# Performance work log

Hardware: AMD Instinct MI355X
Metric: run time of the kernel (lower is better)

## Reference

```python
import jax, jax.numpy as jnp
import numpy as np

B, N_NODE, N_TOK = 8, 512, 8
N_PATHS, PATH_LEN = 256, 64
VOCAB, H = 50000, 256


def gru_dir(x, w_ih, w_hh, b_ih, b_hh):
    # x: [batch, T, H_in] -> [batch, T, H]; PyTorch GRU gate math
    xw = jnp.einsum('bti,gi->btg', x, w_ih) + b_ih  # precompute input-side gates
    h0 = jnp.zeros((x.shape[0], w_hh.shape[1]), x.dtype)
    def step(h, xt):
        gh = h @ w_hh.T + b_hh
        xr, xz, xn = jnp.split(xt, 3, -1)
        hr, hz, hn = jnp.split(gh, 3, -1)
        r = jax.nn.sigmoid(xr + hr)
        z = jax.nn.sigmoid(xz + hz)
        n = jnp.tanh(xn + r * hn)
        h_new = (1.0 - z) * n + z * h
        return h_new, h_new
    _, ys = jax.lax.scan(step, h0, jnp.swapaxes(xw, 0, 1))
    return jnp.swapaxes(ys, 0, 1)


def gru_bidir(x, wf_ih, wf_hh, bf_ih, bf_hh, wb_ih, wb_hh, bb_ih, bb_hh):
    f = gru_dir(x, wf_ih, wf_hh, bf_ih, bf_hh)
    b = jnp.flip(gru_dir(jnp.flip(x, 1), wb_ih, wb_hh, bb_ih, bb_hh), 1)
    return jnp.concatenate([f, b], -1)


def setup_inputs():
    key = jax.random.key(0)
    ks = jax.random.split(key, 18)
    g = lambda k, s: jax.random.normal(k, s, jnp.float32) * 0.06
    return {
        'nodes': jax.random.randint(ks[0], (B, N_NODE, N_TOK), 0, VOCAB),
        'paths': jax.random.randint(ks[1], (B, N_PATHS, PATH_LEN), 0, N_NODE + 1),
        'emb': g(ks[2], (VOCAB, H)),
        'wf_ih': g(ks[3], (3 * H, H)), 'wf_hh': g(ks[4], (3 * H, H)),
        'bf_ih': g(ks[5], (3 * H,)), 'bf_hh': g(ks[6], (3 * H,)),
        'wb_ih': g(ks[7], (3 * H, H)), 'wb_hh': g(ks[8], (3 * H, H)),
        'bb_ih': g(ks[9], (3 * H,)), 'bb_hh': g(ks[10], (3 * H,)),
        'w_transit': g(ks[11], (2 * H, H)), 'b_transit': g(ks[12], (2 * H,)),
        'w_rank': g(ks[13], (2 * H, 2 * H + 1)), 'b_rank': g(ks[14], (2 * H,)),
        'w_h': g(ks[15], (H, 2 * H)), 'b_h': g(ks[16], (H,)),
    }


def reference(nodes, paths, emb, wf_ih, wf_hh, bf_ih, bf_hh, wb_ih, wb_hh, bb_ih, bb_hh, w_transit, b_transit, w_rank, b_rank, w_h, b_h):
    gru = (wf_ih, wf_hh, bf_ih, bf_hh, wb_ih, wb_hh, bb_ih, bb_hh)
    x = jnp.max(emb[nodes], axis=2)                 # [B, N_NODE, H] token max-pool
    base_v = gru_bidir(x, *gru)                     # [B, N_NODE, 2H]
    x_pad = jnp.concatenate([x, jnp.zeros((B, 1, H), x.dtype)], axis=1)
    gathered = jax.vmap(lambda xp, p: xp[p])(x_pad, paths)        # [B, P, L, H]
    nx = gru_bidir(gathered.reshape(B * N_PATHS, PATH_LEN, H), *gru)
    nx = nx.reshape(B, N_PATHS, PATH_LEN, 2 * H)
    # extra rank feature: 1/(path_index+1), broadcast over path positions
    rank = (1.0 / (jnp.arange(N_PATHS, dtype=x.dtype) + 1.0))[None, :, None, None]
    rank = jnp.broadcast_to(rank, (B, N_PATHS, PATH_LEN, 1))
    nx = jnp.concatenate([nx, rank], -1) @ w_rank.T + b_rank      # rank_proj
    p_flat = paths.reshape(B, -1)
    v_flat = nx.reshape(B, N_PATHS * PATH_LEN, 2 * H)
    def pool(pf, vf, xb):
        # scatter-max per node id; id N_NODE is the padding row and is dropped
        vmax = jnp.full((N_NODE + 1, 2 * H), -jnp.inf, vf.dtype).at[pf].max(vf)
        has = jnp.zeros((N_NODE + 1,), bool).at[pf].set(True)
        fallback = xb @ w_transit.T + b_transit
        return jnp.where(has[:N_NODE, None], vmax[:N_NODE], fallback)
    v = jax.vmap(pool)(p_flat, v_flat, x)           # [B, N_NODE, 2H]
    all_v = base_v + v
    last_state = jnp.max(all_v, axis=1) @ w_h.T + b_h             # h_proj branch (GRU -> not tuple)
    return all_v, last_state
```

## Files before the change

### kernel.cpp

```cpp
#include <hip/hip_runtime.h>


#define HH 256
#define NNODE 512
#define PLEN 64

typedef __attribute__((ext_vector_type(8))) short short8;
typedef __attribute__((ext_vector_type(4))) float f32x4;
typedef unsigned short ushort_t;
typedef __attribute__((address_space(1))) const void* gas_t;
typedef __attribute__((address_space(3))) void* las_t;

__device__ __forceinline__ f32x4 mfma16(short8 a, short8 b, f32x4 c) {
    return __builtin_amdgcn_mfma_f32_16x16x32_bf16(a, b, c, 0, 0, 0);
}
__device__ __forceinline__ ushort_t f2bf(float f) {
    unsigned u = __float_as_uint(f);
    u += 0x7fffu + ((u >> 16) & 1u);
    return (ushort_t)(u >> 16);
}
__device__ __forceinline__ float bf2f(ushort_t s) {
    return __uint_as_float(((unsigned)s) << 16);
}
__device__ __forceinline__ float sigm(float x) {
    return __builtin_amdgcn_rcpf(1.f + __expf(-x));
}
__device__ __forceinline__ float tanh_(float x) {
    return 1.f - 2.f * __builtin_amdgcn_rcpf(__expf(2.f * x) + 1.f);
}
__device__ __forceinline__ unsigned fkey(float f) {
    unsigned u = __float_as_uint(f);
    return (u & 0x80000000u) ? ~u : (u | 0x80000000u);
}
__device__ __forceinline__ float fdec(unsigned k) {
    unsigned u = (k & 0x80000000u) ? (k ^ 0x80000000u) : ~k;
    return __uint_as_float(u);
}

__device__ __forceinline__ int xw3_remap(int c) {
    const int dir = c >= 768;
    const int cd = c - dir * 768;
    const int g = cd >> 8, cc = cd & 255;
    const int w2 = cc >> 5, within = cc & 31;
    return dir * 768 + w2 * 96 + (within >> 1) * 6 + g * 2 + (within & 1);
}

__global__ void k_embed(const int* __restrict__ nodes, const float* __restrict__ emb,
                        float* __restrict__ x, ushort_t* __restrict__ xbf)
{
    const int bn = blockIdx.x, h = threadIdx.x;
    const int* nd = nodes + bn * 8;
    float m = -3.4e38f;
#pragma unroll
    for (int k = 0; k < 8; ++k)
        m = fmaxf(m, emb[(size_t)nd[k] * HH + h]);
    x[(size_t)bn * HH + h] = m;
    xbf[(size_t)bn * HH + h] = f2bf(m);
}

__global__ void k_pack(const float* __restrict__ wf_ih, const float* __restrict__ wf_hh,
                       const float* __restrict__ bf_ih, const float* __restrict__ bf_hh,
                       const float* __restrict__ wb_ih, const float* __restrict__ wb_hh,
                       const float* __restrict__ bb_ih, const float* __restrict__ bb_hh,
                       const float* __restrict__ w_rank,
                       ushort_t* __restrict__ whhp, ushort_t* __restrict__ wih_bt,
                       ushort_t* __restrict__ wr_bt, float* __restrict__ rank_l,
                       float* __restrict__ bias2, ushort_t* __restrict__ xw3)
{
    int i = blockIdx.x * 256 + threadIdx.x;
    if (i < 393216) {
        const int e = i & 7, l = (i >> 3) & 63;
        int c = i >> 9;
        const int n = c & 1; c >>= 1;
        const int g = c % 3; c /= 3;
        const int kt = c & 7; c >>= 3;
        const int w2 = c & 7;
        const int dir = c >> 3;
        const float* whh = dir ? wb_hh : wf_hh;
        whhp[i] = f2bf(whh[(g * 256 + w2 * 32 + 2 * (l & 15) + n) * 256 +
                           kt * 32 + (l >> 4) * 8 + e]);
        return;
    }
    i -= 393216;
    if (i < 393216) {
        const int n = i >> 8, k = i & 255;
        const float* wih = (n < 768) ? wf_ih : wb_ih;
        wih_bt[i] = f2bf(wih[(n % 768) * 256 + k]);
        return;
    }
    i -= 393216;
    if (i < 262144) { wr_bt[i] = f2bf(w_rank[(i >> 9) * 513 + (i & 511)]); return; }
    i -= 262144;
    if (i < 512) { rank_l[i] = w_rank[i * 513 + 512]; return; }
    i -= 512;
    if (i < 1536) {
        const int c = i;
        const int dir = c >= 768;
        const int cd = c - dir * 768;
        const int g = cd >> 8;
        const float bi = dir ? bb_ih[cd] : bf_ih[cd];
        const float bh = (g < 2) ? (dir ? bb_hh[cd] : bf_hh[cd]) : 0.f;
        bias2[c] = bi + bh;
        xw3[(size_t)4096 * 1536 + xw3_remap(c)] = f2bf(bi + bh);
    }
}

template<int KD>
__device__ __forceinline__ void gemm_loop(const ushort_t* __restrict__ A,
                                          const ushort_t* __restrict__ Bt,
                                          ushort_t* al, ushort_t* bl,
                                          int bm, int bn, f32x4 acc[4][4])
{
    const int tid = threadIdx.x, w = tid >> 6, l = tid & 63;
    const int lm = l & 15, lh = l >> 4;
    const int wm = w >> 1, wn = w & 1;
    const int lr = l >> 3, lc = (l & 7) * 8;
    for (int k0 = 0; k0 < KD; k0 += 64) {
#pragma unroll
        for (int i = 0; i < 4; ++i) {
            const int c = w * 4 + i;
            const ushort_t* ga = A + (size_t)(bm + c * 8 + lr) * KD + k0 + lc;
            const ushort_t* gb = Bt + (size_t)(bn + c * 8 + lr) * KD + k0 + lc;
            __builtin_amdgcn_global_load_lds((gas_t)ga, (las_t)(al + c * 512), 16, 0, 0);
            __builtin_amdgcn_global_load_lds((gas_t)gb, (las_t)(bl + c * 512), 16, 0, 0);
        }
        __syncthreads();
#pragma unroll
        for (int kt = 0; kt < 2; ++kt) {
            short8 af[4], bfr[4];
            const int ko = kt * 32 + lh * 8;
#pragma unroll
            for (int m = 0; m < 4; ++m)
                af[m] = *(const short8*)(al + (wm * 64 + m * 16 + lm) * 64 + ko);
#pragma unroll
            for (int n = 0; n < 4; ++n)
                bfr[n] = *(const short8*)(bl + (wn * 64 + n * 16 + lm) * 64 + ko);
#pragma unroll
            for (int m = 0; m < 4; ++m)
#pragma unroll
                for (int n = 0; n < 4; ++n)
                    acc[m][n] = mfma16(af[m], bfr[n], acc[m][n]);
        }
        __syncthreads();
    }
}

__global__ void __launch_bounds__(256, 2)
k_gemm_xw(const ushort_t* __restrict__ xbf, const ushort_t* __restrict__ wih_bt,
          const float* __restrict__ bias2, ushort_t* __restrict__ xw3)
{
    __shared__ __align__(16) ushort_t al[128 * 64], bl[128 * 64];
    f32x4 acc[4][4] = {};
    const int bm = blockIdx.y * 128, bn = blockIdx.x * 128;
    gemm_loop<256>(xbf, wih_bt, al, bl, bm, bn, acc);
    const int tid = threadIdx.x, w = tid >> 6, l = tid & 63;
    const int lm = l & 15, lh = l >> 4, wm = w >> 1, wn = w & 1;
#pragma unroll
    for (int m = 0; m < 4; ++m)
#pragma unroll
        for (int rr = 0; rr < 4; ++rr) {
            const int row = bm + wm * 64 + m * 16 + lh * 4 + rr;
#pragma unroll
            for (int n = 0; n < 4; ++n) {
                const int col = bn + wn * 64 + n * 16 + lm;
                xw3[(size_t)row * 1536 + xw3_remap(col)] = f2bf(acc[m][n][rr] + bias2[col]);
            }
        }
}

template<bool IS_BASE>
__device__ __forceinline__ void scan_run(int dir, int sg, int tid,
    const ushort_t* __restrict__ xw3, const ushort_t* __restrict__ whhp,
    const float* __restrict__ bhh, ushort_t (*hl)[8192], const int* idr,
    ushort_t* __restrict__ nx, float* __restrict__ base_v)
{
    const int w = tid >> 6, l = tid & 63;
    const int lm = l & 15, lh = l >> 4;
    const int nsteps = IS_BASE ? NNODE : PLEN;

    short8 Bf[8][3][2];
    {
        const ushort_t* wp = whhp + (size_t)(dir * 8 + w) * 24576 + l * 8;
#pragma unroll
        for (int kt = 0; kt < 8; ++kt)
#pragma unroll
            for (int g = 0; g < 3; ++g)
#pragma unroll
                for (int n = 0; n < 2; ++n) {
                    short8 v = *(const short8*)(wp + (kt * 6 + g * 2 + n) * 512);
                    asm volatile("" : "+a"(v));
                    Bf[kt][g][n] = v;
                }
    }
    const float bn0 = bhh[512 + w * 32 + lm * 2];
    const float bn1 = bhh[512 + w * 32 + lm * 2 + 1];

    __syncthreads();
    for (int i = tid; i < 4096; i += 512) hl[0][i] = 0;
    __syncthreads();

    int cur = 0;
    for (int step = 0; step < nsteps; ++step) {
        const int t = dir ? (nsteps - 1 - step) : step;
        uint3 gv[4];
#pragma unroll
        for (int ri = 0; ri < 4; ++ri) {
            const int sq = lh * 4 + ri;
            const int row = IS_BASE ? ((sq < 8) ? ((sq << 9) + t) : 4096)
                                    : idr[(sq << 6) + t];
            gv[ri] = *(const uint3*)((const char*)xw3 +
                (size_t)row * 3072 + dir * 1536 + w * 192 + lm * 12);
        }
        f32x4 acc[3][2] = {};
        const char* hb = (const char*)hl[cur];
#pragma unroll
        for (int kt = 0; kt < 8; ++kt) {
            const short8 a = *(const short8*)(hb + lm * 512 +
                ((kt * 64 + lh * 16) ^ ((lm & 7) << 4)));
#pragma unroll
            for (int g = 0; g < 3; ++g)
#pragma unroll
                for (int n = 0; n < 2; ++n)
                    acc[g][n] = mfma16(a, Bf[kt][g][n], acc[g][n]);
        }
        ushort_t* hn_ = hl[cur ^ 1];
#pragma unroll
        for (int ri = 0; ri < 4; ++ri) {
            const int sq = lh * 4 + ri;
            const unsigned hv = *(const unsigned*)(hb + sq * 512 +
                ((w * 64 + lm * 4) ^ ((sq & 7) << 4)));
            unsigned hpack = 0;
            float hs0 = 0.f, hs1 = 0.f;
#pragma unroll
            for (int n = 0; n < 2; ++n) {
                const float xr = bf2f((ushort_t)(n ? (gv[ri].x >> 16) : (gv[ri].x & 0xffffu)));
                const float xz = bf2f((ushort_t)(n ? (gv[ri].y >> 16) : (gv[ri].y & 0xffffu)));
                const float xn = bf2f((ushort_t)(n ? (gv[ri].z >> 16) : (gv[ri].z & 0xffffu)));
                const float hov = bf2f((ushort_t)(n ? (hv >> 16) : (hv & 0xffffu)));
                const float rr = sigm(acc[0][n][ri] + xr);
                const float zz = sigm(acc[1][n][ri] + xz);
                const float nn = tanh_(xn + rr * (acc[2][n][ri] + (n ? bn1 : bn0)));
                const float h = (1.f - zz) * nn + zz * hov;
                if (n) hs1 = h; else hs0 = h;
                hpack |= ((unsigned)f2bf(h)) << (n * 16);
            }
            *(unsigned*)((char*)hn_ + sq * 512 + ((w * 64 + lm * 4) ^ ((sq & 7) << 4))) = hpack;
            if (IS_BASE) {
                if (sq < 8)
                    *(float2*)(base_v + ((size_t)(sq * NNODE + t)) * 512 +
                               dir * 256 + w * 32 + lm * 2) = make_float2(hs0, hs1);
            } else {
                *(unsigned*)((char*)nx + (((size_t)((sg * 16 + sq) * PLEN + t)) * 512 +
                    dir * 256 + w * 32 + lm * 2) * 2) = hpack;
            }
        }
        __syncthreads();
        cur ^= 1;
    }
}

__global__ void __launch_bounds__(512)
k_scan(const int* __restrict__ paths, const ushort_t* __restrict__ xw3,
       const ushort_t* __restrict__ whhp,
       const float* __restrict__ bf_hh, const float* __restrict__ bb_hh,
       const ushort_t* __restrict__ wr_bt, const float* __restrict__ b_rank,
       const float* __restrict__ rank_l,
       ushort_t* __restrict__ nx, float* __restrict__ base_v,
       unsigned* __restrict__ keys)
{
    __shared__ __align__(16) ushort_t hl[2][8192];
    __shared__ __align__(16) ushort_t al[12288], bl[12288];
    __shared__ int idr[1024];
    const int tid = threadIdx.x;
    const int w = tid >> 6, l = tid & 63;
    const int lm = l & 15, lh = l >> 4;

    if (blockIdx.x < 2) {
        scan_run<true>((int)blockIdx.x, 0, tid, xw3, whhp,
                       blockIdx.x ? bb_hh : bf_hh, hl, nullptr, nx, base_v);
        return;
    }
    const int sg = (int)blockIdx.x - 2;
    for (int i = tid; i < 1024; i += 512) {
        const int s = sg * 16 + (i >> 6), t = i & 63;
        const int id = paths[(s << 6) + t];
        idr[i] = (id < NNODE) ? (((s >> 8) << 9) + id) : 4096;
    }
    scan_run<false>(0, sg, tid, xw3, whhp, bf_hh, hl, idr, nx, base_v);
    scan_run<false>(1, sg, tid, xw3, whhp, bb_hh, hl, idr, nx, base_v);

    __threadfence_block();
    __syncthreads();
    const int wm = w >> 2, wn = w & 3;
#pragma unroll 1
    for (int job = 0; job < 32; ++job) {
        const int mt = job >> 2, ntile = job & 3;
        const size_t ar0 = (size_t)sg * 1024 + mt * 128;
        const int n0 = ntile * 128;
        f32x4 racc[4][2] = {};
        for (int k0 = 0; k0 < 512; k0 += 64) {
#pragma unroll
            for (int i = 0; i < 2; ++i) {
                const int c = w * 128 + i * 64 + l;
                const int row = c >> 3, j = c & 7;
                const int jp = j ^ (row & 7);
                __builtin_amdgcn_global_load_lds(
                    (gas_t)(nx + (ar0 + row) * 512 + k0 + jp * 8),
                    (las_t)(al + c * 8), 16, 0, 0);
                __builtin_amdgcn_global_load_lds(
                    (gas_t)(wr_bt + (size_t)(n0 + row) * 512 + k0 + jp * 8),
                    (las_t)(bl + c * 8), 16, 0, 0);
            }
            __syncthreads();
#pragma unroll
            for (int kt = 0; kt < 2; ++kt) {
                short8 av[4], bv[2];
#pragma unroll
                for (int m = 0; m < 4; ++m) {
                    const int r = wm * 64 + m * 16 + lm;
                    av[m] = *(const short8*)((const char*)al + r * 128 +
                            ((kt * 64 + lh * 16) ^ ((r & 7) << 4)));
                }
#pragma unroll
                for (int n = 0; n < 2; ++n) {
                    const int r = wn * 32 + n * 16 + lm;
                    bv[n] = *(const short8*)((const char*)bl + r * 128 +
                            ((kt * 64 + lh * 16) ^ ((r & 7) << 4)));
                }
#pragma unroll
                for (int m = 0; m < 4; ++m)
#pragma unroll
                    for (int n = 0; n < 2; ++n)
                        racc[m][n] = mfma16(av[m], bv[n], racc[m][n]);
            }
            __syncthreads();
        }
#pragma unroll
        for (int m = 0; m < 4; ++m)
#pragma unroll
            for (int rr = 0; rr < 4; ++rr) {
                const size_t grow = ar0 + wm * 64 + m * 16 + lh * 4 + rr;
                const int id = paths[grow];
                const float rv = __builtin_amdgcn_rcpf((float)(((grow >> 6) & 255) + 1));
                unsigned* kp = keys + (((grow >> 14) * 513 + id) << 9);
#pragma unroll
                for (int n = 0; n < 2; ++n) {
                    const int col = n0 + wn * 32 + n * 16 + lm;
                    const float v = racc[m][n][rr] + b_rank[col] + rank_l[col] * rv;
                    if (id < NNODE) {
                        const unsigned key = fkey(v);
                        if (key > kp[col]) atomicMax(kp + col, key);
                    }
                }
            }
    }
}

__global__ void k_merge(const unsigned* __restrict__ keys, const float* __restrict__ base_v,
                        const float* __restrict__ x, const float* __restrict__ w_transit,
                        const float* __restrict__ b_transit, float* __restrict__ out0)
{
    const int blk = blockIdx.x;
    const int b = blk >> 9, n = blk & 511;
    const int tid = threadIdx.x;
#pragma unroll
    for (int h = 0; h < 2; ++h) {
        const int o = tid + h * 256;
        const unsigned k = keys[((size_t)(b * 513 + n)) * 512 + o];
        float v;
        if (k) {
            v = fdec(k);
        } else {
            float a = b_transit[o];
            const float* wt = w_transit + o * HH;
            const float* xr = x + ((size_t)(b * NNODE + n)) * HH;
            for (int i = 0; i < HH; ++i) a += xr[i] * wt[i];
            v = a;
        }
        const size_t oi = ((size_t)(b * NNODE + n)) * 512 + o;
        out0[oi] = base_v[oi] + v;
    }
}

__global__ void k_last(const float* __restrict__ out0, const float* __restrict__ w_h,
                       const float* __restrict__ b_h, float* __restrict__ out1)
{
    __shared__ float m[512];
    const int b = blockIdx.x, tid = threadIdx.x;
#pragma unroll
    for (int h = 0; h < 2; ++h) {
        const int o = tid + h * 256;
        float mm = -3.4e38f;
        for (int n = 0; n < NNODE; ++n)
            mm = fmaxf(mm, out0[((size_t)(b * NNODE + n)) * 512 + o]);
        m[o] = mm;
    }
    __syncthreads();
    float a = b_h[tid];
    const float* wr = w_h + tid * 512;
    for (int j = 0; j < 512; ++j) a += m[j] * wr[j];
    out1[b * HH + tid] = a;
}

extern "C" void kernel_launch(void* const* d_in, const int* in_sizes, int n_in,
                              void* d_out, int out_size, void* d_ws, size_t ws_size,
                              hipStream_t stream)
{
    (void)in_sizes; (void)n_in; (void)out_size; (void)ws_size;
    const int* nodes = (const int*)d_in[0];
    const int* paths = (const int*)d_in[1];
    const float* emb = (const float*)d_in[2];
    const float* wf_ih = (const float*)d_in[3];
    const float* wf_hh = (const float*)d_in[4];
    const float* bf_ih = (const float*)d_in[5];
    const float* bf_hh = (const float*)d_in[6];
    const float* wb_ih = (const float*)d_in[7];
    const float* wb_hh = (const float*)d_in[8];
    const float* bb_ih = (const float*)d_in[9];
    const float* bb_hh = (const float*)d_in[10];
    const float* w_transit = (const float*)d_in[11];
    const float* b_transit = (const float*)d_in[12];
    const float* w_rank = (const float*)d_in[13];
    const float* b_rank = (const float*)d_in[14];
    const float* w_h = (const float*)d_in[15];
    const float* b_h = (const float*)d_in[16];

    char* ws = (char*)d_ws;
    float* x = (float*)(ws);
    ushort_t* xbf = (ushort_t*)(ws + 4194304);
    ushort_t* xw3 = (ushort_t*)(ws + 6291456);
    ushort_t* whhp = (ushort_t*)(ws + 18877440);
    ushort_t* wih_bt = (ushort_t*)(ws + 19663872);
    ushort_t* wr_bt = (ushort_t*)(ws + 20450304);
    float* rank_l = (float*)(ws + 20974592);
    float* bias2 = (float*)(ws + 20976640);
    unsigned* keys = (unsigned*)(ws + 20982784);
    float* base_v = (float*)(ws + 29387776);
    ushort_t* nx = (ushort_t*)(ws + 37776384);

    float* out0 = (float*)d_out;
    float* out1 = out0 + 2097152;

    hipMemsetAsync(keys, 0, 8404992, stream);
    k_embed<<<4096, 256, 0, stream>>>(nodes, emb, x, xbf);
    k_pack<<<4104, 256, 0, stream>>>(wf_ih, wf_hh, bf_ih, bf_hh, wb_ih, wb_hh,
                                     bb_ih, bb_hh, w_rank,
                                     whhp, wih_bt, wr_bt, rank_l, bias2, xw3);
    k_gemm_xw<<<dim3(12, 32), 256, 0, stream>>>(xbf, wih_bt, bias2, xw3);
    k_scan<<<130, 512, 0, stream>>>(paths, xw3, whhp, bf_hh, bb_hh, wr_bt,
                                    b_rank, rank_l, nx, base_v, keys);
    k_merge<<<4096, 256, 0, stream>>>(keys, base_v, x, w_transit, b_transit, out0);
    k_last<<<8, 256, 0, stream>>>(out0, w_h, b_h, out1);
}
```

Baseline: 2.026 ms.

## Double scan block to 1024 threads with one output column per lane

The recurrent scan kernel now runs 16 waves per block instead of 8. Each wave owns 16 hidden columns and holds its recurrent weights in VGPRs instead of AGPRs, so each lane computes one column per step rather than two. To suit this, the input-projection output is split into separate r/z-interleaved and n buffers. The xbf buffer now aliases the keys region, so the keys memset is moved after the GEMM that reads xbf. The aim is to halve the per-step serial MFMA and gate work per wave on the latency-bound scan, at the cost of more synchronisation across more waves and scattered 2-byte stores.

```diff
diff --git a/kernel.cpp b/kernel.cpp
--- a/kernel.cpp
+++ b/kernel.cpp
@@ -35,14 +35,6 @@
 __device__ __forceinline__ float fdec(unsigned k) {
     unsigned u = (k & 0x80000000u) ? (k ^ 0x80000000u) : ~k;
     return __uint_as_float(u);
-}
-
-__device__ __forceinline__ int xw3_remap(int c) {
-    const int dir = c >= 768;
-    const int cd = c - dir * 768;
-    const int g = cd >> 8, cc = cd & 255;
-    const int w2 = cc >> 5, within = cc & 31;
-    return dir * 768 + w2 * 96 + (within >> 1) * 6 + g * 2 + (within & 1);
 }
 
 __global__ void k_embed(const int* __restrict__ nodes, const float* __restrict__ emb,
@@ -65,19 +57,19 @@
                        const float* __restrict__ w_rank,
                        ushort_t* __restrict__ whhp, ushort_t* __restrict__ wih_bt,
                        ushort_t* __restrict__ wr_bt, float* __restrict__ rank_l,
-                       float* __restrict__ bias2, ushort_t* __restrict__ xw3)
+                       float* __restrict__ bias2,
+                       ushort_t* __restrict__ xwRZ, ushort_t* __restrict__ xwN)
 {
     int i = blockIdx.x * 256 + threadIdx.x;
     if (i < 393216) {
         const int e = i & 7, l = (i >> 3) & 63;
         int c = i >> 9;
-        const int n = c & 1; c >>= 1;
         const int g = c % 3; c /= 3;
         const int kt = c & 7; c >>= 3;
-        const int w2 = c & 7;
-        const int dir = c >> 3;
+        const int w2 = c & 15;
+        const int dir = c >> 4;
         const float* whh = dir ? wb_hh : wf_hh;
-        whhp[i] = f2bf(whh[(g * 256 + w2 * 32 + 2 * (l & 15) + n) * 256 +
+        whhp[i] = f2bf(whh[(g * 256 + w2 * 16 + (l & 15)) * 256 +
                            kt * 32 + (l >> 4) * 8 + e]);
         return;
     }
@@ -97,11 +89,13 @@
         const int c = i;
         const int dir = c >= 768;
         const int cd = c - dir * 768;
-        const int g = cd >> 8;
+        const int g = cd >> 8, cc = cd & 255;
         const float bi = dir ? bb_ih[cd] : bf_ih[cd];
         const float bh = (g < 2) ? (dir ? bb_hh[cd] : bf_hh[cd]) : 0.f;
         bias2[c] = bi + bh;
-        xw3[(size_t)4096 * 1536 + xw3_remap(c)] = f2bf(bi + bh);
+        const size_t ro = (size_t)(4096 * 2 + dir) * 256 + cc;
+        if (g < 2) xwRZ[ro * 2 + g] = f2bf(bi + bh);
+        else       xwN[ro] = f2bf(bi + bh);
     }
 }
 
@@ -147,7 +141,8 @@
 
 __global__ void __launch_bounds__(256, 2)
 k_gemm_xw(const ushort_t* __restrict__ xbf, const ushort_t* __restrict__ wih_bt,
-          const float* __restrict__ bias2, ushort_t* __restrict__ xw3)
+          const float* __restrict__ bias2,
+          ushort_t* __restrict__ xwRZ, ushort_t* __restrict__ xwN)
 {
     __shared__ __align__(16) ushort_t al[128 * 64], bl[128 * 64];
     f32x4 acc[4][4] = {};
@@ -163,95 +158,90 @@
 #pragma unroll
             for (int n = 0; n < 4; ++n) {
                 const int col = bn + wn * 64 + n * 16 + lm;
-                xw3[(size_t)row * 1536 + xw3_remap(col)] = f2bf(acc[m][n][rr] + bias2[col]);
+                const int dir = col >= 768;
+                const int cd = col - dir * 768;
+                const int g = cd >> 8, cc = cd & 255;
+                const ushort_t v = f2bf(acc[m][n][rr] + bias2[col]);
+                const size_t ro = (size_t)(row * 2 + dir) * 256 + cc;
+                if (g < 2) xwRZ[ro * 2 + g] = v;
+                else       xwN[ro] = v;
             }
         }
 }
 
 template<bool IS_BASE>
 __device__ __forceinline__ void scan_run(int dir, int sg, int tid,
-    const ushort_t* __restrict__ xw3, const ushort_t* __restrict__ whhp,
-    const float* __restrict__ bhh, ushort_t (*hl)[8192], const int* idr,
+    const ushort_t* __restrict__ xwRZ, const ushort_t* __restrict__ xwN,
+    const ushort_t* __restrict__ whhp, const float* __restrict__ bhh,
+    ushort_t (*hl)[8192], const int* idr,
     ushort_t* __restrict__ nx, float* __restrict__ base_v)
 {
     const int w = tid >> 6, l = tid & 63;
     const int lm = l & 15, lh = l >> 4;
+    const int col = w * 16 + lm;
     const int nsteps = IS_BASE ? NNODE : PLEN;
 
-    short8 Bf[8][3][2];
+    short8 Bf[8][3];
     {
-        const ushort_t* wp = whhp + (size_t)(dir * 8 + w) * 24576 + l * 8;
+        const ushort_t* wp = whhp + (size_t)(dir * 16 + w) * 12288 + l * 8;
 #pragma unroll
         for (int kt = 0; kt < 8; ++kt)
 #pragma unroll
-            for (int g = 0; g < 3; ++g)
-#pragma unroll
-                for (int n = 0; n < 2; ++n) {
-                    short8 v = *(const short8*)(wp + (kt * 6 + g * 2 + n) * 512);
-                    asm volatile("" : "+a"(v));
-                    Bf[kt][g][n] = v;
-                }
-    }
-    const float bn0 = bhh[512 + w * 32 + lm * 2];
-    const float bn1 = bhh[512 + w * 32 + lm * 2 + 1];
+            for (int g = 0; g < 3; ++g) {
+                short8 v = *(const short8*)(wp + (kt * 3 + g) * 512);
+                asm volatile("" : "+v"(v));
+                Bf[kt][g] = v;
+            }
+    }
+    const float bn_ = bhh[512 + col];
 
     __syncthreads();
-    for (int i = tid; i < 4096; i += 512) hl[0][i] = 0;
+    for (int i = tid; i < 4096; i += 1024) hl[0][i] = 0;
     __syncthreads();
 
     int cur = 0;
     for (int step = 0; step < nsteps; ++step) {
         const int t = dir ? (nsteps - 1 - step) : step;
-        uint3 gv[4];
+        unsigned grz[4]; ushort_t gn[4];
 #pragma unroll
         for (int ri = 0; ri < 4; ++ri) {
             const int sq = lh * 4 + ri;
             const int row = IS_BASE ? ((sq < 8) ? ((sq << 9) + t) : 4096)
                                     : idr[(sq << 6) + t];
-            gv[ri] = *(const uint3*)((const char*)xw3 +
-                (size_t)row * 3072 + dir * 1536 + w * 192 + lm * 12);
-        }
-        f32x4 acc[3][2] = {};
+            const size_t ro = (size_t)(row * 2 + dir) * 256 + col;
+            grz[ri] = *(const unsigned*)(xwRZ + ro * 2);
+            gn[ri] = xwN[ro];
+        }
+        f32x4 acc[3] = {};
         const char* hb = (const char*)hl[cur];
 #pragma unroll
         for (int kt = 0; kt < 8; ++kt) {
             const short8 a = *(const short8*)(hb + lm * 512 +
                 ((kt * 64 + lh * 16) ^ ((lm & 7) << 4)));
-#pragma unroll
-            for (int g = 0; g < 3; ++g)
-#pragma unroll
-                for (int n = 0; n < 2; ++n)
-                    acc[g][n] = mfma16(a, Bf[kt][g][n], acc[g][n]);
+            acc[0] = mfma16(a, Bf[kt][0], acc[0]);
+            acc[1] = mfma16(a, Bf[kt][1], acc[1]);
+            acc[2] = mfma16(a, Bf[kt][2], acc[2]);
         }
         ushort_t* hn_ = hl[cur ^ 1];
 #pragma unroll
         for (int ri = 0; ri < 4; ++ri) {
             const int sq = lh * 4 + ri;
-            const unsigned hv = *(const unsigned*)(hb + sq * 512 +
-                ((w * 64 + lm * 4) ^ ((sq & 7) << 4)));
-            unsigned hpack = 0;
-            float hs0 = 0.f, hs1 = 0.f;
-#pragma unroll
-            for (int n = 0; n < 2; ++n) {
-                const float xr = bf2f((ushort_t)(n ? (gv[ri].x >> 16) : (gv[ri].x & 0xffffu)));
-                const float xz = bf2f((ushort_t)(n ? (gv[ri].y >> 16) : (gv[ri].y & 0xffffu)));
-                const float xn = bf2f((ushort_t)(n ? (gv[ri].z >> 16) : (gv[ri].z & 0xffffu)));
-                const float hov = bf2f((ushort_t)(n ? (hv >> 16) : (hv & 0xffffu)));
-                const float rr = sigm(acc[0][n][ri] + xr);
-                const float zz = sigm(acc[1][n][ri] + xz);
-                const float nn = tanh_(xn + rr * (acc[2][n][ri] + (n ? bn1 : bn0)));
-                const float h = (1.f - zz) * nn + zz * hov;
-                if (n) hs1 = h; else hs0 = h;
-                hpack |= ((unsigned)f2bf(h)) << (n * 16);
-            }
-            *(unsigned*)((char*)hn_ + sq * 512 + ((w * 64 + lm * 4) ^ ((sq & 7) << 4))) = hpack;
+            const int hoff = sq * 512 + ((col * 2) ^ ((sq & 7) << 4));
+            const float hov = bf2f(*(const ushort_t*)(hb + hoff));
+            const float xr = bf2f((ushort_t)(grz[ri] & 0xffffu));
+            const float xz = bf2f((ushort_t)(grz[ri] >> 16));
+            const float xn = bf2f(gn[ri]);
+            const float rr = sigm(acc[0][ri] + xr);
+            const float zz = sigm(acc[1][ri] + xz);
+            const float nn = tanh_(xn + rr * (acc[2][ri] + bn_));
+            const float h = (1.f - zz) * nn + zz * hov;
+            const ushort_t h16 = f2bf(h);
+            *(ushort_t*)((char*)hn_ + hoff) = h16;
             if (IS_BASE) {
                 if (sq < 8)
-                    *(float2*)(base_v + ((size_t)(sq * NNODE + t)) * 512 +
-                               dir * 256 + w * 32 + lm * 2) = make_float2(hs0, hs1);
+                    base_v[((size_t)(sq * NNODE + t)) * 512 + dir * 256 + col] = h;
             } else {
-                *(unsigned*)((char*)nx + (((size_t)((sg * 16 + sq) * PLEN + t)) * 512 +
-                    dir * 256 + w * 32 + lm * 2) * 2) = hpack;
+                nx[((size_t)((sg * 16 + sq) * PLEN + t)) * 512 + dir * 256 + col] = h16;
             }
         }
         __syncthreads();
@@ -259,8 +249,9 @@
     }
 }
 
-__global__ void __launch_bounds__(512)
-k_scan(const int* __restrict__ paths, const ushort_t* __restrict__ xw3,
+__global__ void __launch_bounds__(1024, 1)
+k_scan(const int* __restrict__ paths,
+       const ushort_t* __restrict__ xwRZ, const ushort_t* __restrict__ xwN,
        const ushort_t* __restrict__ whhp,
        const float* __restrict__ bf_hh, const float* __restrict__ bb_hh,
        const ushort_t* __restrict__ wr_bt, const float* __restrict__ b_rank,
@@ -276,18 +267,18 @@
     const int lm = l & 15, lh = l >> 4;
 
     if (blockIdx.x < 2) {
-        scan_run<true>((int)blockIdx.x, 0, tid, xw3, whhp,
+        scan_run<true>((int)blockIdx.x, 0, tid, xwRZ, xwN, whhp,
                        blockIdx.x ? bb_hh : bf_hh, hl, nullptr, nx, base_v);
         return;
     }
     const int sg = (int)blockIdx.x - 2;
-    for (int i = tid; i < 1024; i += 512) {
-        const int s = sg * 16 + (i >> 6), t = i & 63;
+    {
+        const int s = sg * 16 + (tid >> 6), t = tid & 63;
         const int id = paths[(s << 6) + t];
-        idr[i] = (id < NNODE) ? (((s >> 8) << 9) + id) : 4096;
-    }
-    scan_run<false>(0, sg, tid, xw3, whhp, bf_hh, hl, idr, nx, base_v);
-    scan_run<false>(1, sg, tid, xw3, whhp, bb_hh, hl, idr, nx, base_v);
+        idr[tid] = (id < NNODE) ? (((s >> 8) << 9) + id) : 4096;
+    }
+    scan_run<false>(0, sg, tid, xwRZ, xwN, whhp, bf_hh, hl, idr, nx, base_v);
+    scan_run<false>(1, sg, tid, xwRZ, xwN, whhp, bb_hh, hl, idr, nx, base_v);
 
     __threadfence_block();
     __syncthreads();
@@ -297,27 +288,25 @@
         const int mt = job >> 2, ntile = job & 3;
         const size_t ar0 = (size_t)sg * 1024 + mt * 128;
         const int n0 = ntile * 128;
-        f32x4 racc[4][2] = {};
+        f32x4 racc[2][2] = {};
         for (int k0 = 0; k0 < 512; k0 += 64) {
-#pragma unroll
-            for (int i = 0; i < 2; ++i) {
-                const int c = w * 128 + i * 64 + l;
-                const int row = c >> 3, j = c & 7;
+            {
+                const int row = tid >> 3, j = tid & 7;
                 const int jp = j ^ (row & 7);
                 __builtin_amdgcn_global_load_lds(
                     (gas_t)(nx + (ar0 + row) * 512 + k0 + jp * 8),
-                    (las_t)(al + c * 8), 16, 0, 0);
+                    (las_t)(al + tid * 8), 16, 0, 0);
                 __builtin_amdgcn_global_load_lds(
                     (gas_t)(wr_bt + (size_t)(n0 + row) * 512 + k0 + jp * 8),
-                    (las_t)(bl + c * 8), 16, 0, 0);
+                    (las_t)(bl + tid * 8), 16, 0, 0);
             }
             __syncthreads();
 #pragma unroll
             for (int kt = 0; kt < 2; ++kt) {
-                short8 av[4], bv[2];
-#pragma unroll
-                for (int m = 0; m < 4; ++m) {
-                    const int r = wm * 64 + m * 16 + lm;
+                short8 av[2], bv[2];
+#pragma unroll
+                for (int m = 0; m < 2; ++m) {
+                    const int r = wm * 32 + m * 16 + lm;
                     av[m] = *(const short8*)((const char*)al + r * 128 +
                             ((kt * 64 + lh * 16) ^ ((r & 7) << 4)));
                 }
@@ -328,7 +317,7 @@
                             ((kt * 64 + lh * 16) ^ ((r & 7) << 4)));
                 }
 #pragma unroll
-                for (int m = 0; m < 4; ++m)
+                for (int m = 0; m < 2; ++m)
 #pragma unroll
                     for (int n = 0; n < 2; ++n)
                         racc[m][n] = mfma16(av[m], bv[n], racc[m][n]);
@@ -336,10 +325,10 @@
             __syncthreads();
         }
 #pragma unroll
-        for (int m = 0; m < 4; ++m)
+        for (int m = 0; m < 2; ++m)
 #pragma unroll
             for (int rr = 0; rr < 4; ++rr) {
-                const size_t grow = ar0 + wm * 64 + m * 16 + lh * 4 + rr;
+                const size_t grow = ar0 + wm * 32 + m * 16 + lh * 4 + rr;
                 const int id = paths[grow];
                 const float rv = __builtin_amdgcn_rcpf((float)(((grow >> 6) & 255) + 1));
                 unsigned* kp = keys + (((grow >> 14) * 513 + id) << 9);
@@ -427,28 +416,29 @@
 
     char* ws = (char*)d_ws;
     float* x = (float*)(ws);
-    ushort_t* xbf = (ushort_t*)(ws + 4194304);
-    ushort_t* xw3 = (ushort_t*)(ws + 6291456);
-    ushort_t* whhp = (ushort_t*)(ws + 18877440);
-    ushort_t* wih_bt = (ushort_t*)(ws + 19663872);
-    ushort_t* wr_bt = (ushort_t*)(ws + 20450304);
-    float* rank_l = (float*)(ws + 20974592);
-    float* bias2 = (float*)(ws + 20976640);
-    unsigned* keys = (unsigned*)(ws + 20982784);
-    float* base_v = (float*)(ws + 29387776);
-    ushort_t* nx = (ushort_t*)(ws + 37776384);
+    ushort_t* xwRZ = (ushort_t*)(ws + 4194304);
+    ushort_t* xwN = (ushort_t*)(ws + 12584960);
+    ushort_t* whhp = (ushort_t*)(ws + 16780288);
+    ushort_t* wih_bt = (ushort_t*)(ws + 17566720);
+    ushort_t* wr_bt = (ushort_t*)(ws + 18353152);
+    float* rank_l = (float*)(ws + 18877440);
+    float* bias2 = (float*)(ws + 18879488);
+    unsigned* keys = (unsigned*)(ws + 18885632);
+    ushort_t* xbf = (ushort_t*)(ws + 18885632);
+    float* base_v = (float*)(ws + 27290624);
+    ushort_t* nx = (ushort_t*)(ws + 35679232);
 
     float* out0 = (float*)d_out;
     float* out1 = out0 + 2097152;
 
-    hipMemsetAsync(keys, 0, 8404992, stream);
     k_embed<<<4096, 256, 0, stream>>>(nodes, emb, x, xbf);
     k_pack<<<4104, 256, 0, stream>>>(wf_ih, wf_hh, bf_ih, bf_hh, wb_ih, wb_hh,
                                      bb_ih, bb_hh, w_rank,
-                                     whhp, wih_bt, wr_bt, rank_l, bias2, xw3);
-    k_gemm_xw<<<dim3(12, 32), 256, 0, stream>>>(xbf, wih_bt, bias2, xw3);
-    k_scan<<<130, 512, 0, stream>>>(paths, xw3, whhp, bf_hh, bb_hh, wr_bt,
-                                    b_rank, rank_l, nx, base_v, keys);
+                                     whhp, wih_bt, wr_bt, rank_l, bias2, xwRZ, xwN);
+    k_gemm_xw<<<dim3(12, 32), 256, 0, stream>>>(xbf, wih_bt, bias2, xwRZ, xwN);
+    hipMemsetAsync(keys, 0, 8404992, stream);
+    k_scan<<<130, 1024, 0, stream>>>(paths, xwRZ, xwN, whhp, bf_hh, bb_hh, wr_bt,
+                                     b_rank, rank_l, nx, base_v, keys);
     k_merge<<<4096, 256, 0, stream>>>(keys, base_v, x, w_transit, b_transit, out0);
     k_last<<<8, 256, 0, stream>>>(out0, w_h, b_h, out1);
 }
```

After: 2.041 ms. Within noise of the previous version (+0.7%).
